# Kernel tuning notes

Hardware: AMD Instinct MI355X
Metric: run time of the kernel (lower is better)

The kernel has to match this reference:

```python
import jax, jax.numpy as jnp
import numpy as np

B, E, H = 128, 512, 1024
NEG = -1000000.0


def setup_inputs() -> dict:
    key = jax.random.key(0)
    ks = jax.random.split(key, 10)
    inv = 1.0 / np.sqrt(H)
    return {
        "query": jax.random.normal(ks[0], (B, H), jnp.float32),
        "keys": jax.random.normal(ks[1], (B, E, H), jnp.float32),
        "entity_size": jax.random.randint(ks[2], (B,), 0, E + 1, jnp.int32),
        "mention_score": jax.random.normal(ks[3], (B,), jnp.float32),
        # scorer params (torch Linear(2H->H) then Linear(H->1)), stored transposed
        "W1": jax.random.normal(ks[4], (2 * H, H), jnp.float32) * inv,
        "b1": jnp.zeros((H,), jnp.float32),
        "W2": jax.random.normal(ks[5], (H, 1), jnp.float32) * inv,
        "b2": jnp.zeros((1,), jnp.float32),
        "null_address": jax.random.normal(ks[6], (H,), jnp.float32) * inv,
        "new_address": jax.random.normal(ks[7], (H,), jnp.float32) * inv,
    }


def reference(query, keys, entity_size, mention_score, W1, b1, W2, b2, null_address, new_address):
    b, e, h = keys.shape
    # prepend null address, append new address -> [B, E+2, H]
    null = jnp.broadcast_to(null_address, (b, 1, h))
    new = jnp.broadcast_to(new_address, (b, 1, h))
    keys_full = jnp.concatenate([null, keys, new], axis=1)
    q = jnp.broadcast_to(query[:, None, :], (b, e + 2, h))
    qk = jnp.concatenate([q, keys_full], axis=-1)  # [B, E+2, 2H]
    hid = jax.nn.gelu(jnp.einsum("bsd,dh->bsh", qk, W1) + b1, approximate=False)
    scores = (jnp.einsum("bsh,ho->bso", hid, W2) + b2)[..., 0]  # [B, E+2]
    # mention score with sign flip on the null slot (column 0)
    inv_mask = jnp.ones((e + 2,), scores.dtype).at[0].set(-1.0)
    scores = scores + mention_score[:, None] * inv_mask[None, :]
    # mask out slots entity_size[b]+1 .. E (exclusive of the final 'new' slot)
    idx = jnp.arange(e + 2)
    mask = jnp.where((idx[None, :] >= entity_size[:, None] + 1) & (idx[None, :] <= e), NEG, 0.0).astype(scores.dtype)
    return scores + mask
```

## Files before the change

kernel.cpp:

```cpp
#include <hip/hip_runtime.h>
#include <hip/hip_bf16.h>

#define B_ 128
#define E_ 512
#define H_ 1024
#define S_ 514
#define NEGV -1000000.0f

typedef __attribute__((ext_vector_type(8))) short bf16x8;
typedef __attribute__((ext_vector_type(4))) short s16x4;
typedef __attribute__((ext_vector_type(4))) float f32x4;

__device__ __forceinline__ short f2bf(float f) {
  unsigned u = __builtin_bit_cast(unsigned, f);
  return (short)((u + 0x8000u) >> 16);
}

__device__ __forceinline__ float gelu_f(float x) {
  return 0.5f * x * (1.0f + erff(x * 0.7071067811865475f));
}

__global__ void prep_q1(const float* __restrict__ query, const float* __restrict__ W1,
                        const float* __restrict__ b1, const float* __restrict__ nulla,
                        const float* __restrict__ newa, float* __restrict__ Q1,
                        float* __restrict__ N1, float* __restrict__ A1) {
  __shared__ float vec[H_];
  int bid = blockIdx.x;
  int rowIdx = bid >> 2;
  int h = (bid & 3) * 256 + threadIdx.x;
  const float* src;
  int woff;
  if (rowIdx < B_)      { src = query + (size_t)rowIdx * H_; woff = 0; }
  else if (rowIdx == B_){ src = nulla; woff = H_; }
  else                  { src = newa;  woff = H_; }
  for (int i = threadIdx.x; i < H_; i += 256) vec[i] = src[i];
  __syncthreads();
  float acc = (rowIdx < B_) ? b1[h] : 0.f;
  const float* wp = W1 + (size_t)woff * H_ + h;
  #pragma unroll 8
  for (int d = 0; d < H_; ++d) acc += vec[d] * wp[(size_t)d * H_];
  if (rowIdx < B_)       Q1[rowIdx * H_ + h] = acc;
  else if (rowIdx == B_) N1[h] = acc;
  else                   A1[h] = acc;
}

__global__ void transpose_w1k(const float* __restrict__ W1, short* __restrict__ w1kT) {
  __shared__ float tb[64][65];
  int k0 = (blockIdx.x & 15) * 64;
  int n0 = (blockIdx.x >> 4) * 64;
  int x = threadIdx.x & 63;
  int ty = threadIdx.x >> 6;
  #pragma unroll
  for (int i = 0; i < 16; ++i) {
    int row = i * 4 + ty;
    tb[row][x] = W1[(size_t)(H_ + k0 + row) * H_ + n0 + x];
  }
  __syncthreads();
  #pragma unroll
  for (int i = 0; i < 16; ++i) {
    int row = i * 4 + ty;
    w1kT[(size_t)(n0 + row) * H_ + k0 + x] = f2bf(tb[x][row]);
  }
}

__global__ void finalize_base(const int* __restrict__ es, const float* __restrict__ mention,
                              const float* __restrict__ W2, const float* __restrict__ b2,
                              const float* __restrict__ Q1, const float* __restrict__ N1,
                              const float* __restrict__ A1, float* __restrict__ scores) {
  int b = blockIdx.x;
  int t = threadIdx.x;
  float b2v = b2[0], mv = mention[b];
  int esz = es[b];
  for (int s = t; s < S_; s += 256) {
    float base = b2v + (s == 0 ? -mv : mv);
    if (s >= esz + 1 && s <= E_) base += NEGV;
    scores[b * S_ + s] = base;
  }
  float sum0 = 0.f, sum1 = 0.f;
  for (int h = t; h < H_; h += 256) {
    float q = Q1[b * H_ + h], w = W2[h];
    sum0 += gelu_f(q + N1[h]) * w;
    sum1 += gelu_f(q + A1[h]) * w;
  }
  #pragma unroll
  for (int m = 32; m > 0; m >>= 1) { sum0 += __shfl_xor(sum0, m); sum1 += __shfl_xor(sum1, m); }
  __shared__ float red0[4], red1[4];
  int lanei = t & 63, wdi = t >> 6;
  if (lanei == 0) { red0[wdi] = sum0; red1[wdi] = sum1; }
  __syncthreads();
  if (t == 0) {
    scores[b * S_ + 0]      += red0[0] + red0[1] + red0[2] + red0[3];
    scores[b * S_ + S_ - 1] += red1[0] + red1[1] + red1[2] + red1[3];
  }
}

#define BM 128
#define BN 128
#define BK 64
#define LDT 72

__global__ __launch_bounds__(256, 2) void gemm_epilogue(
    const float* __restrict__ keys, const short* __restrict__ w1kT,
    const float* __restrict__ Q1, const float* __restrict__ W2,
    float* __restrict__ scores) {
  __shared__ short As[BM * LDT];
  __shared__ short Bs[BN * LDT];

  int bid = blockIdx.x;
  int cpx = gridDim.x >> 3;
  bid = (bid & 7) * cpx + (bid >> 3);
  int tileM = bid >> 3;
  int tileN = bid & 7;
  int row0 = tileM * BM;
  int col0 = tileN * BN;

  int t = threadIdx.x;
  int lane = t & 63;
  int wid = t >> 6;
  int wr = wid >> 1, wc = wid & 1;
  int l15 = lane & 15, lHi = lane >> 4;

  int asr = t >> 4;
  int asc = (t & 15) * 4;
  int bsr = t >> 3;
  int bsc = (t & 7) * 8;

  const float* aBase = keys + (size_t)(row0 + asr) * H_ + asc;
  const short* bBase = w1kT + (size_t)(col0 + bsr) * H_ + bsc;

  f32x4 aReg[8];
  bf16x8 bReg[4];
  f32x4 acc[4][4];
  #pragma unroll
  for (int m = 0; m < 4; ++m)
    #pragma unroll
    for (int n = 0; n < 4; ++n) acc[m][n] = (f32x4){0.f, 0.f, 0.f, 0.f};

  #pragma unroll
  for (int p = 0; p < 8; ++p) aReg[p] = *(const f32x4*)(aBase + (size_t)p * 16 * H_);
  #pragma unroll
  for (int p = 0; p < 4; ++p) bReg[p] = *(const bf16x8*)(bBase + (size_t)p * 32 * H_);

  for (int k0 = 0; k0 < H_; k0 += BK) {
    __syncthreads();
    #pragma unroll
    for (int p = 0; p < 8; ++p) {
      s16x4 v;
      #pragma unroll
      for (int j = 0; j < 4; ++j) v[j] = f2bf(aReg[p][j]);
      *(s16x4*)&As[(p * 16 + asr) * LDT + asc] = v;
    }
    #pragma unroll
    for (int p = 0; p < 4; ++p)
      *(bf16x8*)&Bs[(p * 32 + bsr) * LDT + bsc] = bReg[p];
    __syncthreads();
    if (k0 + BK < H_) {
      #pragma unroll
      for (int p = 0; p < 8; ++p) aReg[p] = *(const f32x4*)(aBase + (size_t)p * 16 * H_ + k0 + BK);
      #pragma unroll
      for (int p = 0; p < 4; ++p) bReg[p] = *(const bf16x8*)(bBase + (size_t)p * 32 * H_ + k0 + BK);
    }
    #pragma unroll
    for (int kk = 0; kk < 2; ++kk) {
      bf16x8 af[4], bfv[4];
      #pragma unroll
      for (int m = 0; m < 4; ++m)
        af[m] = *(const bf16x8*)&As[(wr * 64 + m * 16 + l15) * LDT + kk * 32 + lHi * 8];
      #pragma unroll
      for (int n = 0; n < 4; ++n)
        bfv[n] = *(const bf16x8*)&Bs[(wc * 64 + n * 16 + l15) * LDT + kk * 32 + lHi * 8];
      #pragma unroll
      for (int m = 0; m < 4; ++m)
        #pragma unroll
        for (int n = 0; n < 4; ++n)
          acc[m][n] = __builtin_amdgcn_mfma_f32_16x16x32_bf16(af[m], bfv[n], acc[m][n], 0, 0, 0);
    }
  }

  int bIdx = row0 >> 9;
  float q1v[4], w2v[4];
  #pragma unroll
  for (int n = 0; n < 4; ++n) {
    int col = col0 + wc * 64 + n * 16 + l15;
    q1v[n] = Q1[bIdx * H_ + col];
    w2v[n] = W2[col];
  }
  #pragma unroll
  for (int m = 0; m < 4; ++m) {
    float part[4] = {0.f, 0.f, 0.f, 0.f};
    #pragma unroll
    for (int n = 0; n < 4; ++n)
      #pragma unroll
      for (int i = 0; i < 4; ++i)
        part[i] += gelu_f(acc[m][n][i] + q1v[n]) * w2v[n];
    #pragma unroll
    for (int i = 0; i < 4; ++i) {
      float v = part[i];
      v += __shfl_xor(v, 1);
      v += __shfl_xor(v, 2);
      v += __shfl_xor(v, 4);
      v += __shfl_xor(v, 8);
      if (l15 == 0) {
        int row = row0 + wr * 64 + m * 16 + lHi * 4 + i;
        int s = (row & 511) + 1;
        atomicAdd(&scores[bIdx * S_ + s], v);
      }
    }
  }
}

extern "C" void kernel_launch(void* const* d_in, const int* in_sizes, int n_in,
                              void* d_out, int out_size, void* d_ws, size_t ws_size,
                              hipStream_t stream) {
  const float* query   = (const float*)d_in[0];
  const float* keys    = (const float*)d_in[1];
  const int*   esz     = (const int*)d_in[2];
  const float* mention = (const float*)d_in[3];
  const float* W1      = (const float*)d_in[4];
  const float* b1      = (const float*)d_in[5];
  const float* W2      = (const float*)d_in[6];
  const float* b2      = (const float*)d_in[7];
  const float* nulla   = (const float*)d_in[8];
  const float* newa    = (const float*)d_in[9];
  float* scores = (float*)d_out;

  short* w1kT = (short*)d_ws;
  float* Q1   = (float*)((char*)d_ws + (size_t)2 * 1024 * 1024);
  float* N1   = Q1 + (size_t)B_ * H_;
  float* A1   = N1 + H_;

  prep_q1<<<520, 256, 0, stream>>>(query, W1, b1, nulla, newa, Q1, N1, A1);
  transpose_w1k<<<256, 256, 0, stream>>>(W1, w1kT);
  finalize_base<<<B_, 256, 0, stream>>>(esz, mention, W2, b2, Q1, N1, A1, scores);
  gemm_epilogue<<<4096, 256, 0, stream>>>(keys, w1kT, Q1, W2, scores);
}
```

Before: 645.1 us.

## Split-K query projection with atomics; direct-to-LDS B loads with XOR swizzle

The per-row query projection (one thread per output, serial loop over 1024 inputs) is replaced by an init kernel that seeds the outputs with the bias. A split-K kernel then computes 8 rows per block with vectorized W1 loads and accumulates into Q1/N1/A1 with atomics. In the main GEMM, the bf16 weight tiles are now loaded straight into LDS with global_load_lds instead of being staged through registers. The padded LDS layout is replaced by an XOR-swizzled one to avoid bank conflicts. This adds a kernel launch and makes the float sums order-dependent, and it drops the register prefetch of B, so B loads are no longer overlapped with the previous tile's compute.

```diff
diff --git a/kernel.cpp b/kernel.cpp
--- a/kernel.cpp
+++ b/kernel.cpp
@@ -11,6 +11,9 @@
 typedef __attribute__((ext_vector_type(4))) short s16x4;
 typedef __attribute__((ext_vector_type(4))) float f32x4;
 
+typedef __attribute__((address_space(1))) const void* gptr_t;
+typedef __attribute__((address_space(3))) void* lptr_t;
+
 __device__ __forceinline__ short f2bf(float f) {
   unsigned u = __builtin_bit_cast(unsigned, f);
   return (short)((u + 0x8000u) >> 16);
@@ -20,28 +23,77 @@
   return 0.5f * x * (1.0f + erff(x * 0.7071067811865475f));
 }
 
-__global__ void prep_q1(const float* __restrict__ query, const float* __restrict__ W1,
-                        const float* __restrict__ b1, const float* __restrict__ nulla,
-                        const float* __restrict__ newa, float* __restrict__ Q1,
+__global__ void init_q1(const float* __restrict__ b1, float* __restrict__ Q1,
                         float* __restrict__ N1, float* __restrict__ A1) {
-  __shared__ float vec[H_];
+  int b = blockIdx.x;
+  int t = threadIdx.x;
+  if (b < B_) {
+    f32x4 v = *(const f32x4*)(b1 + t * 4);
+    *(f32x4*)(Q1 + (size_t)b * H_ + t * 4) = v;
+  } else if (b == B_) {
+    *(f32x4*)(N1 + t * 4) = (f32x4){0.f, 0.f, 0.f, 0.f};
+  } else {
+    *(f32x4*)(A1 + t * 4) = (f32x4){0.f, 0.f, 0.f, 0.f};
+  }
+}
+
+#define RPB 8
+__global__ void prep2(const float* __restrict__ query, const float* __restrict__ W1,
+                      const float* __restrict__ nulla, const float* __restrict__ newa,
+                      float* __restrict__ Q1, float* __restrict__ N1, float* __restrict__ A1) {
   int bid = blockIdx.x;
-  int rowIdx = bid >> 2;
-  int h = (bid & 3) * 256 + threadIdx.x;
-  const float* src;
-  int woff;
-  if (rowIdx < B_)      { src = query + (size_t)rowIdx * H_; woff = 0; }
-  else if (rowIdx == B_){ src = nulla; woff = H_; }
-  else                  { src = newa;  woff = H_; }
-  for (int i = threadIdx.x; i < H_; i += 256) vec[i] = src[i];
+  int rg = bid >> 4;
+  int dc = bid & 15;
+  int t = threadIdx.x;
+  bool special = (rg == 16);
+  int woff = special ? H_ : 0;
+
+  __shared__ float vec[RPB][64];
+  {
+    int r = t >> 6, dd = t & 63;
+    #pragma unroll
+    for (int rr = 0; rr < 2; ++rr) {
+      int row = r + rr * 4;
+      float v = 0.f;
+      if (!special) v = query[(size_t)(rg * RPB + row) * H_ + dc * 64 + dd];
+      else if (row == 0) v = nulla[dc * 64 + dd];
+      else if (row == 1) v = newa[dc * 64 + dd];
+      vec[row][dd] = v;
+    }
+  }
   __syncthreads();
-  float acc = (rowIdx < B_) ? b1[h] : 0.f;
-  const float* wp = W1 + (size_t)woff * H_ + h;
-  #pragma unroll 8
-  for (int d = 0; d < H_; ++d) acc += vec[d] * wp[(size_t)d * H_];
-  if (rowIdx < B_)       Q1[rowIdx * H_ + h] = acc;
-  else if (rowIdx == B_) N1[h] = acc;
-  else                   A1[h] = acc;
+
+  const float* wp = W1 + (size_t)(woff + dc * 64) * H_ + t * 4;
+  f32x4 acc[RPB];
+  #pragma unroll
+  for (int r = 0; r < RPB; ++r) acc[r] = (f32x4){0.f, 0.f, 0.f, 0.f};
+
+  #pragma unroll 4
+  for (int dd = 0; dd < 64; ++dd) {
+    f32x4 w = *(const f32x4*)(wp + (size_t)dd * H_);
+    #pragma unroll
+    for (int r = 0; r < RPB; ++r) {
+      float v = vec[r][dd];
+      acc[r][0] += v * w[0]; acc[r][1] += v * w[1];
+      acc[r][2] += v * w[2]; acc[r][3] += v * w[3];
+    }
+  }
+
+  if (!special) {
+    #pragma unroll
+    for (int r = 0; r < RPB; ++r) {
+      float* dst = Q1 + (size_t)(rg * RPB + r) * H_ + t * 4;
+      atomicAdd(dst + 0, acc[r][0]); atomicAdd(dst + 1, acc[r][1]);
+      atomicAdd(dst + 2, acc[r][2]); atomicAdd(dst + 3, acc[r][3]);
+    }
+  } else {
+    float* d0 = N1 + t * 4;
+    atomicAdd(d0 + 0, acc[0][0]); atomicAdd(d0 + 1, acc[0][1]);
+    atomicAdd(d0 + 2, acc[0][2]); atomicAdd(d0 + 3, acc[0][3]);
+    float* d1 = A1 + t * 4;
+    atomicAdd(d1 + 0, acc[1][0]); atomicAdd(d1 + 1, acc[1][1]);
+    atomicAdd(d1 + 2, acc[1][2]); atomicAdd(d1 + 3, acc[1][3]);
+  }
 }
 
 __global__ void transpose_w1k(const float* __restrict__ W1, short* __restrict__ w1kT) {
@@ -94,25 +146,24 @@
   }
 }
 
-#define BM 128
-#define BN 128
-#define BK 64
-#define LDT 72
-
-__global__ __launch_bounds__(256, 2) void gemm_epilogue(
-    const float* __restrict__ keys, const short* __restrict__ w1kT,
+#define GBM 128
+#define GBN 128
+#define GBK 64
+
+__global__ __launch_bounds__(256, 2) void gemm_fused(
+    const float* __restrict__ keys, const short* __restrict__ Bm,
     const float* __restrict__ Q1, const float* __restrict__ W2,
     float* __restrict__ scores) {
-  __shared__ short As[BM * LDT];
-  __shared__ short Bs[BN * LDT];
+  __shared__ short As[GBM * GBK];
+  __shared__ short Bs[GBN * GBK];
 
   int bid = blockIdx.x;
   int cpx = gridDim.x >> 3;
   bid = (bid & 7) * cpx + (bid >> 3);
   int tileM = bid >> 3;
   int tileN = bid & 7;
-  int row0 = tileM * BM;
-  int col0 = tileN * BN;
+  int row0 = tileM * GBM;
+  int col0 = tileN * GBN;
 
   int t = threadIdx.x;
   int lane = t & 63;
@@ -122,14 +173,15 @@
 
   int asr = t >> 4;
   int asc = (t & 15) * 4;
-  int bsr = t >> 3;
-  int bsc = (t & 7) * 8;
-
   const float* aBase = keys + (size_t)(row0 + asr) * H_ + asc;
-  const short* bBase = w1kT + (size_t)(col0 + bsr) * H_ + bsc;
+  char* aWr = (char*)As + asr * 128 + ((((t & 15) * 8)) ^ ((asr & 7) << 4));
+
+  int srcRow = lane >> 3;
+  int srcColE = ((lane & 7) ^ (lane >> 3)) << 3;
+  const short* bSrc = Bm + (size_t)(col0 + wid * 32 + srcRow) * H_ + srcColE;
+  short* bDst = Bs + (wid * 4) * 512;
 
   f32x4 aReg[8];
-  bf16x8 bReg[4];
   f32x4 acc[4][4];
   #pragma unroll
   for (int m = 0; m < 4; ++m)
@@ -138,42 +190,44 @@
 
   #pragma unroll
   for (int p = 0; p < 8; ++p) aReg[p] = *(const f32x4*)(aBase + (size_t)p * 16 * H_);
-  #pragma unroll
-  for (int p = 0; p < 4; ++p) bReg[p] = *(const bf16x8*)(bBase + (size_t)p * 32 * H_);
-
-  for (int k0 = 0; k0 < H_; k0 += BK) {
+
+  int swz = (l15 & 7) << 4;
+  const char* aRd = (const char*)As + (wr * 64 + l15) * 128;
+  const char* bRd = (const char*)Bs + (wc * 64 + l15) * 128;
+
+  for (int k0 = 0; k0 < H_; k0 += GBK) {
     __syncthreads();
     #pragma unroll
     for (int p = 0; p < 8; ++p) {
       s16x4 v;
       #pragma unroll
       for (int j = 0; j < 4; ++j) v[j] = f2bf(aReg[p][j]);
-      *(s16x4*)&As[(p * 16 + asr) * LDT + asc] = v;
-    }
-    #pragma unroll
-    for (int p = 0; p < 4; ++p)
-      *(bf16x8*)&Bs[(p * 32 + bsr) * LDT + bsc] = bReg[p];
+      *(s16x4*)(aWr + p * 2048) = v;
+    }
+    #pragma unroll
+    for (int i = 0; i < 4; ++i)
+      __builtin_amdgcn_global_load_lds((gptr_t)(bSrc + (size_t)i * 8 * H_ + k0),
+                                       (lptr_t)(bDst + i * 512), 16, 0, 0);
     __syncthreads();
-    if (k0 + BK < H_) {
-      #pragma unroll
-      for (int p = 0; p < 8; ++p) aReg[p] = *(const f32x4*)(aBase + (size_t)p * 16 * H_ + k0 + BK);
-      #pragma unroll
-      for (int p = 0; p < 4; ++p) bReg[p] = *(const bf16x8*)(bBase + (size_t)p * 32 * H_ + k0 + BK);
+    if (k0 + GBK < H_) {
+      #pragma unroll
+      for (int p = 0; p < 8; ++p)
+        aReg[p] = *(const f32x4*)(aBase + (size_t)p * 16 * H_ + k0 + GBK);
     }
     #pragma unroll
     for (int kk = 0; kk < 2; ++kk) {
-      bf16x8 af[4], bfv[4];
+      bf16x8 af[4], bv[4];
       #pragma unroll
       for (int m = 0; m < 4; ++m)
-        af[m] = *(const bf16x8*)&As[(wr * 64 + m * 16 + l15) * LDT + kk * 32 + lHi * 8];
+        af[m] = *(const bf16x8*)(aRd + m * 2048 + (((kk << 6) | (lHi << 4)) ^ swz));
       #pragma unroll
       for (int n = 0; n < 4; ++n)
-        bfv[n] = *(const bf16x8*)&Bs[(wc * 64 + n * 16 + l15) * LDT + kk * 32 + lHi * 8];
+        bv[n] = *(const bf16x8*)(bRd + n * 2048 + (((kk << 6) | (lHi << 4)) ^ swz));
       #pragma unroll
       for (int m = 0; m < 4; ++m)
         #pragma unroll
         for (int n = 0; n < 4; ++n)
-          acc[m][n] = __builtin_amdgcn_mfma_f32_16x16x32_bf16(af[m], bfv[n], acc[m][n], 0, 0, 0);
+          acc[m][n] = __builtin_amdgcn_mfma_f32_16x16x32_bf16(af[m], bv[n], acc[m][n], 0, 0, 0);
     }
   }
 
@@ -224,13 +278,15 @@
   const float* newa    = (const float*)d_in[9];
   float* scores = (float*)d_out;
 
+  const size_t w1kTBytes = (size_t)H_ * H_ * 2;
   short* w1kT = (short*)d_ws;
-  float* Q1   = (float*)((char*)d_ws + (size_t)2 * 1024 * 1024);
+  float* Q1   = (float*)((char*)d_ws + w1kTBytes);
   float* N1   = Q1 + (size_t)B_ * H_;
   float* A1   = N1 + H_;
 
-  prep_q1<<<520, 256, 0, stream>>>(query, W1, b1, nulla, newa, Q1, N1, A1);
+  init_q1<<<130, 256, 0, stream>>>(b1, Q1, N1, A1);
+  prep2<<<272, 256, 0, stream>>>(query, W1, nulla, newa, Q1, N1, A1);
   transpose_w1k<<<256, 256, 0, stream>>>(W1, w1kT);
   finalize_base<<<B_, 256, 0, stream>>>(esz, mention, W2, b2, Q1, N1, A1, scores);
-  gemm_epilogue<<<4096, 256, 0, stream>>>(keys, w1kT, Q1, W2, scores);
-}
+  gemm_fused<<<4096, 256, 0, stream>>>(keys, w1kT, Q1, W2, scores);
+}
```

Result: no change. 643.8 us (-0.2%).
